# Optimization experiments

Measured on AMD Instinct MI355X. Metric: run time of the kernel, lower is better.

## Reference

```python
import jax, jax.numpy as jnp
import numpy as np

B, N, F = 4, 1024, 512        # batch, tokens, features
H, D = 8, 64                  # heads, attention_dim (= value dim here)
E = 16                        # edge feature dim
LN_EPS = 1e-5


def setup_inputs() -> dict:
    key = jax.random.key(0)
    ks = jax.random.split(key, 9)
    receiver_input = jax.random.normal(ks[0], (B, N, F), dtype=jnp.float32)
    edge_features = jax.random.normal(ks[1], (B, N, N, E), dtype=jnp.float32)
    mask = (jax.random.uniform(ks[2], (B, N, N)) > 0.5).astype(jnp.float32)
    s = 1.0 / np.sqrt(F)
    Wq = jax.random.normal(ks[3], (F, H * D), dtype=jnp.float32) * s
    Wk = jax.random.normal(ks[4], (F, H * D), dtype=jnp.float32) * s
    Wv = jax.random.normal(ks[5], (F, H * D), dtype=jnp.float32) * s
    We = jax.random.normal(ks[6], (E, H), dtype=jnp.float32) * (1.0 / np.sqrt(E))
    Wo = jax.random.normal(ks[7], (H * D, H * D), dtype=jnp.float32) * (1.0 / np.sqrt(H * D))
    ln_scale = jnp.ones((F,), dtype=jnp.float32)
    ln_offset = jnp.zeros((F,), dtype=jnp.float32)
    return {
        "receiver_input": receiver_input, "edge_features": edge_features,
        "mask": mask, "ln_scale": ln_scale, "ln_offset": ln_offset,
        "Wq": Wq, "Wk": Wk, "Wv": Wv, "We": We, "Wo": Wo,
    }


def _layer_norm(x, scale, offset):
    mu = jnp.mean(x, axis=-1, keepdims=True)
    var = jnp.var(x, axis=-1, keepdims=True)
    return (x - mu) * jax.lax.rsqrt(var + LN_EPS) * scale + offset


def reference(receiver_input, edge_features, mask, ln_scale, ln_offset, Wq, Wk, Wv, We, Wo):
    r = _layer_norm(receiver_input, ln_scale, ln_offset)   # sender = receiver (self-attn)
    q = (r @ Wq).reshape(B, N, H, D)
    k = (r @ Wk).reshape(B, N, H, D)
    v = (r @ Wv).reshape(B, N, H, D)
    # logits [b, i, j, h]; edge bias added BEFORE softmax (over senders j = axis -2)
    logits = jnp.einsum("bihf,bjhf->bijh", q, k) + edge_features @ We
    w = jax.nn.softmax(logits, axis=-2)
    w = w * mask[..., None]                                 # post-softmax mask multiply
    out = jnp.einsum("bijh,bjhv->bihv", w, v)
    out = out.reshape(B, N, H * D) * (1.0 / jnp.sqrt(jnp.float32(D)))
    out = out @ Wo
    out = out + receiver_input                              # residual (shapes match: F == H*D)
    return out
```

## Files before the change

### kernel.cpp

```cpp
#include <hip/hip_runtime.h>

#define BB 4
#define NN 1024
#define FF 512
#define HH 8
#define DD 64
#define EE 16

typedef unsigned short u16;
typedef __attribute__((ext_vector_type(8))) short     bf16x8;
typedef __attribute__((ext_vector_type(8))) unsigned short u16x8;
typedef __attribute__((ext_vector_type(4))) float     f32x4;

#define MFMA(a,b,c) __builtin_amdgcn_mfma_f32_16x16x32_bf16((a),(b),(c),0,0,0)

static __device__ __forceinline__ u16 f2bf(float f){
  unsigned u = __float_as_uint(f);
  unsigned r = (u + 0x7FFFu + ((u >> 16) & 1u)) >> 16;
  return (u16)r;
}
static __device__ __forceinline__ float bf2f(u16 h){
  return __uint_as_float(((unsigned)h) << 16);
}
static __device__ __forceinline__ void gld16(const void* g, void* l){
  __builtin_amdgcn_global_load_lds((const __attribute__((address_space(1))) unsigned int*)g,
                                   (__attribute__((address_space(3))) unsigned int*)l, 16, 0, 0);
}

__global__ __launch_bounds__(256) void k_wsplit(
    const float* __restrict__ Wq, const float* __restrict__ Wk,
    const float* __restrict__ Wv, const float* __restrict__ Wo,
    u16* __restrict__ WhT, u16* __restrict__ WlT, u16* __restrict__ WoT){
  __shared__ float tile[32][33];
  int bid = blockIdx.x, t = threadIdx.x;
  int isA = bid < 768;
  int tb  = isA ? bid : bid - 768;
  int nct = isA ? 48 : 16;
  int ct = tb % nct, ft = tb / nct;
  int c0 = ct * 32, f0 = ft * 32;
  #pragma unroll
  for (int r4 = 0; r4 < 4; r4++){
    int fl = (t >> 5) * 4 + r4, cl = t & 31;
    int f = f0 + fl, c = c0 + cl;
    float v;
    if (isA){
      const float* W = (c < 512) ? Wq : ((c < 1024) ? Wk : Wv);
      v = W[f * 512 + (c & 511)];
    } else {
      v = Wo[f * 512 + c];
    }
    tile[fl][cl] = v;
  }
  __syncthreads();
  #pragma unroll
  for (int r4 = 0; r4 < 4; r4++){
    int cl = (t >> 5) * 4 + r4, fl = t & 31;
    float v = tile[fl][cl];
    int c = c0 + cl, f = f0 + fl;
    if (isA){
      u16 hi = f2bf(v);
      WhT[c * 512 + f] = hi;
      WlT[c * 512 + f] = f2bf(v - bf2f(hi));
    } else {
      WoT[c * 512 + f] = f2bf(v);
    }
  }
}

__global__ __launch_bounds__(256) void k_ln(
    const float* __restrict__ x, const float* __restrict__ gamma,
    const float* __restrict__ beta, u16* __restrict__ rh, u16* __restrict__ rl){
  int row  = blockIdx.x * 4 + (threadIdx.x >> 6);
  int lane = threadIdx.x & 63;
  const float* px = x + (size_t)row * 512 + lane * 8;
  float4 a = *(const float4*)px;
  float4 b = *(const float4*)(px + 4);
  float v[8] = {a.x,a.y,a.z,a.w,b.x,b.y,b.z,b.w};
  float s = 0.f, q = 0.f;
  #pragma unroll
  for (int j = 0; j < 8; j++){ s += v[j]; q += v[j]*v[j]; }
  #pragma unroll
  for (int m = 1; m < 64; m <<= 1){ s += __shfl_xor(s, m, 64); q += __shfl_xor(q, m, 64); }
  float mean = s * (1.f/512.f);
  float var  = q * (1.f/512.f) - mean * mean;
  float rstd = rsqrtf(var + 1e-5f);
  float4 ga = *(const float4*)(gamma + lane*8);
  float4 gb = *(const float4*)(gamma + lane*8 + 4);
  float4 b0 = *(const float4*)(beta  + lane*8);
  float4 b1 = *(const float4*)(beta  + lane*8 + 4);
  float gs[8] = {ga.x,ga.y,ga.z,ga.w,gb.x,gb.y,gb.z,gb.w};
  float bs[8] = {b0.x,b0.y,b0.z,b0.w,b1.x,b1.y,b1.z,b1.w};
  u16x8 hv, lv;
  #pragma unroll
  for (int j = 0; j < 8; j++){
    float r = (v[j] - mean) * rstd * gs[j] + bs[j];
    u16 hi = f2bf(r);
    hv[j] = hi;
    lv[j] = f2bf(r - bf2f(hi));
  }
  *(u16x8*)(rh + (size_t)row * 512 + lane * 8) = hv;
  *(u16x8*)(rl + (size_t)row * 512 + lane * 8) = lv;
}

__global__ __launch_bounds__(256) void k_qkv(
    const u16* __restrict__ rh, const u16* __restrict__ rl,
    const u16* __restrict__ WhT, const u16* __restrict__ WlT,
    u16* __restrict__ qh, u16* __restrict__ ql,
    u16* __restrict__ kh, u16* __restrict__ kl, u16* __restrict__ vT){
  __shared__ u16 Ah[128*32], Al[128*32], Bh[128*32], Bl[128*32];
  int bid = blockIdx.x;
  int mt = bid & 31, nt = bid >> 5;
  int m0 = mt << 7,  n0 = nt << 7;
  int t = threadIdx.x, lane = t & 63, w = t >> 6;
  int wm = (w >> 1) << 6, wn = (w & 1) << 6;
  int fr = lane & 15, g = lane >> 4;
  f32x4 acc[4][4];
  #pragma unroll
  for (int i = 0; i < 4; i++)
    #pragma unroll
    for (int j = 0; j < 4; j++) acc[i][j] = (f32x4){0.f,0.f,0.f,0.f};

  for (int k0 = 0; k0 < 512; k0 += 32){
    #pragma unroll
    for (int q = 0; q < 2; q++){
      int c = ((q << 2) + w) * 64 + lane;
      int row = c >> 2, part = c & 3;
      int ldso = ((q << 2) + w) * 512;
      gld16(rh  + (size_t)(m0+row)*512 + k0 + part*8, &Ah[ldso]);
      gld16(rl  + (size_t)(m0+row)*512 + k0 + part*8, &Al[ldso]);
      gld16(WhT + (size_t)(n0+row)*512 + k0 + part*8, &Bh[ldso]);
      gld16(WlT + (size_t)(n0+row)*512 + k0 + part*8, &Bl[ldso]);
    }
    __syncthreads();
    bf16x8 a_h[4], a_l[4], b_h[4], b_l[4];
    #pragma unroll
    for (int mi = 0; mi < 4; mi++){
      int off = (wm + mi*16 + fr)*32 + g*8;
      a_h[mi] = *(const bf16x8*)&Ah[off];
      a_l[mi] = *(const bf16x8*)&Al[off];
    }
    #pragma unroll
    for (int ni = 0; ni < 4; ni++){
      int off = (wn + ni*16 + fr)*32 + g*8;
      b_h[ni] = *(const bf16x8*)&Bh[off];
      b_l[ni] = *(const bf16x8*)&Bl[off];
    }
    #pragma unroll
    for (int mi = 0; mi < 4; mi++)
      #pragma unroll
      for (int ni = 0; ni < 4; ni++){
        acc[mi][ni] = MFMA(a_h[mi], b_h[ni], acc[mi][ni]);
        acc[mi][ni] = MFMA(a_h[mi], b_l[ni], acc[mi][ni]);
        acc[mi][ni] = MFMA(a_l[mi], b_h[ni], acc[mi][ni]);
      }
    __syncthreads();
  }
  #pragma unroll
  for (int mi = 0; mi < 4; mi++)
    #pragma unroll
    for (int ni = 0; ni < 4; ni++)
      #pragma unroll
      for (int r = 0; r < 4; r++){
        int gm = m0 + wm + mi*16 + g*4 + r;
        int gc = n0 + wn + ni*16 + fr;
        float vv = acc[mi][ni][r];
        int b = gm >> 10, i = gm & 1023;
        int mat = gc >> 9, h = (gc >> 6) & 7, d = gc & 63;
        size_t idx = ((size_t)((b << 3) + h) * 1024 + i) * 64 + d;
        if (mat == 0){
          u16 hi = f2bf(vv); qh[idx] = hi; ql[idx] = f2bf(vv - bf2f(hi));
        } else if (mat == 1){
          u16 hi = f2bf(vv); kh[idx] = hi; kl[idx] = f2bf(vv - bf2f(hi));
        } else {
          vT[((size_t)((b << 3) + h) * 64 + d) * 1024 + i] = f2bf(vv);
        }
      }
}

__global__ __launch_bounds__(512) void k_attn(
    const float* __restrict__ edge, const float* __restrict__ mask,
    const float* __restrict__ We,
    const u16* __restrict__ qh, const u16* __restrict__ ql,
    const u16* __restrict__ kh, const u16* __restrict__ kl,
    const u16* __restrict__ vT, u16* __restrict__ AO){
  __shared__ float We_s[128];
  __shared__ float bias_s[8][16*33];
  __shared__ float mask_s[16*33];
  __shared__ u16   pm_s[8][16*40];

  int bid = blockIdx.x;
  int b = bid >> 6, i0 = (bid & 63) << 4;
  int t = threadIdx.x, lane = t & 63, w = t >> 6;
  int fr = lane & 15, g = lane >> 4;
  if (t < 128) We_s[t] = We[t];

  size_t qb = ((size_t)((b << 3) + w) * 1024 + i0 + fr) * 64 + g * 8;
  bf16x8 qfh0 = *(const bf16x8*)(qh + qb);
  bf16x8 qfh1 = *(const bf16x8*)(qh + qb + 32);
  bf16x8 qfl0 = *(const bf16x8*)(ql + qb);
  bf16x8 qfl1 = *(const bf16x8*)(ql + qb + 32);

  f32x4 oacc[4];
  #pragma unroll
  for (int vf = 0; vf < 4; vf++) oacc[vf] = (f32x4){0.f,0.f,0.f,0.f};
  float mrun[4], den[4];
  #pragma unroll
  for (int r = 0; r < 4; r++){ mrun[r] = -3e38f; den[r] = 0.f; }

  int pi = t >> 5, pj = t & 31;
  const float* ebase = edge + (size_t)(b*1024 + i0 + pi) * 16384 + (size_t)pj * 16;
  const float* mbase = mask + (size_t)(b*1024 + i0 + pi) * 1024 + pj;
  __syncthreads();

  float4 e0 = *(const float4*)(ebase);
  float4 e1 = *(const float4*)(ebase + 4);
  float4 e2 = *(const float4*)(ebase + 8);
  float4 e3 = *(const float4*)(ebase + 12);
  float  mval = *mbase;

  #pragma unroll 1
  for (int jt = 0; jt < 32; jt++){
    int j0 = jt << 5;
    float ef[16] = {e0.x,e0.y,e0.z,e0.w, e1.x,e1.y,e1.z,e1.w,
                    e2.x,e2.y,e2.z,e2.w, e3.x,e3.y,e3.z,e3.w};
    float bias[8] = {0.f,0.f,0.f,0.f,0.f,0.f,0.f,0.f};
    #pragma unroll
    for (int e = 0; e < 16; e++){
      float ev = ef[e];
      #pragma unroll
      for (int h = 0; h < 8; h++) bias[h] += ev * We_s[e*8 + h];
    }
    #pragma unroll
    for (int h = 0; h < 8; h++) bias_s[h][pi*33 + pj] = bias[h];
    mask_s[pi*33 + pj] = mval;
    __syncthreads();

    if (jt < 31){
      const float* ep = ebase + (size_t)(j0 + 32) * 16;
      e0 = *(const float4*)(ep);
      e1 = *(const float4*)(ep + 4);
      e2 = *(const float4*)(ep + 8);
      e3 = *(const float4*)(ep + 12);
      mval = mbase[j0 + 32];
    }

    size_t kb0 = ((size_t)((b << 3) + w) * 1024 + j0 + fr) * 64 + g * 8;
    size_t kb1 = kb0 + 16 * 64;
    bf16x8 kfh00 = *(const bf16x8*)(kh + kb0);
    bf16x8 kfh01 = *(const bf16x8*)(kh + kb0 + 32);
    bf16x8 kfh10 = *(const bf16x8*)(kh + kb1);
    bf16x8 kfh11 = *(const bf16x8*)(kh + kb1 + 32);
    bf16x8 kfl00 = *(const bf16x8*)(kl + kb0);
    bf16x8 kfl01 = *(const bf16x8*)(kl + kb0 + 32);
    bf16x8 kfl10 = *(const bf16x8*)(kl + kb1);
    bf16x8 kfl11 = *(const bf16x8*)(kl + kb1 + 32);

    f32x4 lg0 = (f32x4){0.f,0.f,0.f,0.f};
    f32x4 lg1 = (f32x4){0.f,0.f,0.f,0.f};
    lg0 = MFMA(qfh0, kfh00, lg0); lg0 = MFMA(qfh1, kfh01, lg0);
    lg0 = MFMA(qfh0, kfl00, lg0); lg0 = MFMA(qfh1, kfl01, lg0);
    lg0 = MFMA(qfl0, kfh00, lg0); lg0 = MFMA(qfl1, kfh01, lg0);
    lg1 = MFMA(qfh0, kfh10, lg1); lg1 = MFMA(qfh1, kfh11, lg1);
    lg1 = MFMA(qfh0, kfl10, lg1); lg1 = MFMA(qfh1, kfl11, lg1);
    lg1 = MFMA(qfl0, kfh10, lg1); lg1 = MFMA(qfl1, kfh11, lg1);

    float tm[4];
    #pragma unroll
    for (int r = 0; r < 4; r++){
      int row = g*4 + r;
      lg0[r] += bias_s[w][row*33 + fr];
      lg1[r] += bias_s[w][row*33 + 16 + fr];
      tm[r] = fmaxf(lg0[r], lg1[r]);
    }
    #pragma unroll
    for (int mk = 1; mk < 16; mk <<= 1){
      #pragma unroll
      for (int r = 0; r < 4; r++) tm[r] = fmaxf(tm[r], __shfl_xor(tm[r], mk, 16));
    }
    float p0[4], p1[4], scl[4], ps[4];
    #pragma unroll
    for (int r = 0; r < 4; r++){
      float nm = fmaxf(mrun[r], tm[r]);
      scl[r] = exp2f((mrun[r] - nm) * 1.44269504089f);
      mrun[r] = nm;
      p0[r] = exp2f((lg0[r] - nm) * 1.44269504089f);
      p1[r] = exp2f((lg1[r] - nm) * 1.44269504089f);
      ps[r] = p0[r] + p1[r];
    }
    #pragma unroll
    for (int mk = 1; mk < 16; mk <<= 1){
      #pragma unroll
      for (int r = 0; r < 4; r++) ps[r] += __shfl_xor(ps[r], mk, 16);
    }
    #pragma unroll
    for (int r = 0; r < 4; r++) den[r] = den[r] * scl[r] + ps[r];
    #pragma unroll
    for (int vf = 0; vf < 4; vf++)
      #pragma unroll
      for (int r = 0; r < 4; r++) oacc[vf][r] *= scl[r];

    #pragma unroll
    for (int r = 0; r < 4; r++){
      int row = g*4 + r;
      pm_s[w][row*40 + fr]      = f2bf(p0[r] * mask_s[row*33 + fr]);
      pm_s[w][row*40 + 16 + fr] = f2bf(p1[r] * mask_s[row*33 + 16 + fr]);
    }
    asm volatile("s_waitcnt lgkmcnt(0)" ::: "memory");
    bf16x8 pa = *(const bf16x8*)&pm_s[w][fr*40 + g*8];
    #pragma unroll
    for (int vf = 0; vf < 4; vf++){
      const u16* vp = vT + ((size_t)((b << 3) + w) * 64 + vf*16 + fr) * 1024 + j0 + g*8;
      bf16x8 vfr = *(const bf16x8*)vp;
      oacc[vf] = MFMA(pa, vfr, oacc[vf]);
    }
    __syncthreads();
  }

  float id[4];
  #pragma unroll
  for (int r = 0; r < 4; r++) id[r] = 0.125f / den[r];
  #pragma unroll
  for (int vf = 0; vf < 4; vf++)
    #pragma unroll
    for (int r = 0; r < 4; r++){
      int row = g*4 + r, v = vf*16 + fr;
      AO[((size_t)(b*1024 + i0 + row)) * 512 + w*64 + v] = f2bf(oacc[vf][r] * id[r]);
    }
}

__global__ __launch_bounds__(256) void k_out(
    const u16* __restrict__ AO, const u16* __restrict__ WoT,
    const float* __restrict__ x, float* __restrict__ out){
  __shared__ u16 As[64*32], Bs[128*32];
  int bid = blockIdx.x;
  int mt = bid & 63, nt = bid >> 6;
  int m0 = mt << 6, n0 = nt << 7;
  int t = threadIdx.x, lane = t & 63, w = t >> 6;
  int wm = (w >> 1) << 5, wn = (w & 1) << 6;
  int fr = lane & 15, g = lane >> 4;
  f32x4 acc[2][4];
  #pragma unroll
  for (int i = 0; i < 2; i++)
    #pragma unroll
    for (int j = 0; j < 4; j++) acc[i][j] = (f32x4){0.f,0.f,0.f,0.f};

  for (int k0 = 0; k0 < 512; k0 += 32){
    {
      int row = t >> 2, part = t & 3;
      gld16(AO + (size_t)(m0+row)*512 + k0 + part*8, &As[w*512]);
    }
    #pragma unroll
    for (int q = 0; q < 2; q++){
      int c = ((q << 2) + w) * 64 + lane;
      int row = c >> 2, part = c & 3;
      gld16(WoT + (size_t)(n0+row)*512 + k0 + part*8, &Bs[((q<<2)+w)*512]);
    }
    __syncthreads();
    bf16x8 af[2], bf_[4];
    #pragma unroll
    for (int mi = 0; mi < 2; mi++) af[mi]  = *(const bf16x8*)&As[(wm + mi*16 + fr)*32 + g*8];
    #pragma unroll
    for (int ni = 0; ni < 4; ni++) bf_[ni] = *(const bf16x8*)&Bs[(wn + ni*16 + fr)*32 + g*8];
    #pragma unroll
    for (int mi = 0; mi < 2; mi++)
      #pragma unroll
      for (int ni = 0; ni < 4; ni++)
        acc[mi][ni] = MFMA(af[mi], bf_[ni], acc[mi][ni]);
    __syncthreads();
  }
  #pragma unroll
  for (int mi = 0; mi < 2; mi++)
    #pragma unroll
    for (int ni = 0; ni < 4; ni++)
      #pragma unroll
      for (int r = 0; r < 4; r++){
        size_t gm = m0 + wm + mi*16 + g*4 + r;
        size_t gn = n0 + wn + ni*16 + fr;
        out[gm*512 + gn] = acc[mi][ni][r] + x[gm*512 + gn];
      }
}

extern "C" void kernel_launch(void* const* d_in, const int* in_sizes, int n_in,
                              void* d_out, int out_size, void* d_ws, size_t ws_size,
                              hipStream_t stream){
  const float* xin   = (const float*)d_in[0];
  const float* edge  = (const float*)d_in[1];
  const float* mask  = (const float*)d_in[2];
  const float* gamma = (const float*)d_in[3];
  const float* beta  = (const float*)d_in[4];
  const float* Wq    = (const float*)d_in[5];
  const float* Wk    = (const float*)d_in[6];
  const float* Wv    = (const float*)d_in[7];
  const float* We    = (const float*)d_in[8];
  const float* Wo    = (const float*)d_in[9];
  float* out = (float*)d_out;

  u16* p   = (u16*)d_ws;
  u16* WhT = p;                 p += 1536*512;
  u16* WlT = p;                 p += 1536*512;
  u16* WoT = p;                 p += 512*512;
  u16* rh  = p;                 p += 4096*512;
  u16* rl  = p;                 p += 4096*512;
  u16* qh  = p;                 p += 2097152;
  u16* ql  = p;                 p += 2097152;
  u16* kh  = p;                 p += 2097152;
  u16* kl  = p;                 p += 2097152;
  u16* vT  = p;                 p += 2097152;
  u16* AO  = p;                 p += 2097152;

  k_wsplit<<<1024, 256, 0, stream>>>(Wq, Wk, Wv, Wo, WhT, WlT, WoT);
  k_ln    <<<1024, 256, 0, stream>>>(xin, gamma, beta, rh, rl);
  k_qkv   <<<384,  256, 0, stream>>>(rh, rl, WhT, WlT, qh, ql, kh, kl, vT);
  k_attn  <<<256,  512, 0, stream>>>(edge, mask, We, qh, ql, kh, kl, vT, AO);
  k_out   <<<256,  256, 0, stream>>>(AO, WoT, xin, out);
}
```

Before: 215.1 us.

## Split attention over sender dimension with flash-decoding partials and combine kernel

The attention kernel now splits the 1024 senders into four chunks, launching four times as many blocks, and each writes a partial normalized output plus its running max and denominator. A new combine kernel merges the four partials with log-sum-exp weighting and writes the final attention output. It also adds an occupancy hint to launch bounds, interleaves the two independent MFMA chains, and reuses the workspace by aliasing the partials over the dead LN and weight buffers. The goal is better CU occupancy with 256 CUs, at the cost of an extra launch, extra partial traffic, and bf16 rounding of the partials.

```diff
diff --git a/kernel.cpp b/kernel.cpp
--- a/kernel.cpp
+++ b/kernel.cpp
@@ -177,19 +177,22 @@
       }
 }
 
-__global__ __launch_bounds__(512) void k_attn(
+__global__ __launch_bounds__(512, 6) void k_attn(
     const float* __restrict__ edge, const float* __restrict__ mask,
     const float* __restrict__ We,
     const u16* __restrict__ qh, const u16* __restrict__ ql,
     const u16* __restrict__ kh, const u16* __restrict__ kl,
-    const u16* __restrict__ vT, u16* __restrict__ AO){
+    const u16* __restrict__ vT, u16* __restrict__ part_o,
+    float2* __restrict__ part_md){
   __shared__ float We_s[128];
   __shared__ float bias_s[8][16*33];
   __shared__ float mask_s[16*33];
   __shared__ u16   pm_s[8][16*40];
 
   int bid = blockIdx.x;
-  int b = bid >> 6, i0 = (bid & 63) << 4;
+  int s  = bid & 3;
+  int i0 = ((bid >> 2) & 63) << 4;
+  int b  = bid >> 8;
   int t = threadIdx.x, lane = t & 63, w = t >> 6;
   int fr = lane & 15, g = lane >> 4;
   if (t < 128) We_s[t] = We[t];
@@ -208,8 +211,8 @@
   for (int r = 0; r < 4; r++){ mrun[r] = -3e38f; den[r] = 0.f; }
 
   int pi = t >> 5, pj = t & 31;
-  const float* ebase = edge + (size_t)(b*1024 + i0 + pi) * 16384 + (size_t)pj * 16;
-  const float* mbase = mask + (size_t)(b*1024 + i0 + pi) * 1024 + pj;
+  const float* ebase = edge + ((size_t)(b*1024 + i0 + pi) * 1024 + s*256 + pj) * 16;
+  const float* mbase = mask + (size_t)(b*1024 + i0 + pi) * 1024 + s*256 + pj;
   __syncthreads();
 
   float4 e0 = *(const float4*)(ebase);
@@ -219,8 +222,8 @@
   float  mval = *mbase;
 
   #pragma unroll 1
-  for (int jt = 0; jt < 32; jt++){
-    int j0 = jt << 5;
+  for (int jt = 0; jt < 8; jt++){
+    int j0 = s*256 + (jt << 5);
     float ef[16] = {e0.x,e0.y,e0.z,e0.w, e1.x,e1.y,e1.z,e1.w,
                     e2.x,e2.y,e2.z,e2.w, e3.x,e3.y,e3.z,e3.w};
     float bias[8] = {0.f,0.f,0.f,0.f,0.f,0.f,0.f,0.f};
@@ -235,13 +238,13 @@
     mask_s[pi*33 + pj] = mval;
     __syncthreads();
 
-    if (jt < 31){
-      const float* ep = ebase + (size_t)(j0 + 32) * 16;
+    if (jt < 7){
+      const float* ep = ebase + (size_t)((jt + 1) << 5) * 16;
       e0 = *(const float4*)(ep);
       e1 = *(const float4*)(ep + 4);
       e2 = *(const float4*)(ep + 8);
       e3 = *(const float4*)(ep + 12);
-      mval = mbase[j0 + 32];
+      mval = mbase[(jt + 1) << 5];
     }
 
     size_t kb0 = ((size_t)((b << 3) + w) * 1024 + j0 + fr) * 64 + g * 8;
@@ -257,12 +260,12 @@
 
     f32x4 lg0 = (f32x4){0.f,0.f,0.f,0.f};
     f32x4 lg1 = (f32x4){0.f,0.f,0.f,0.f};
-    lg0 = MFMA(qfh0, kfh00, lg0); lg0 = MFMA(qfh1, kfh01, lg0);
-    lg0 = MFMA(qfh0, kfl00, lg0); lg0 = MFMA(qfh1, kfl01, lg0);
-    lg0 = MFMA(qfl0, kfh00, lg0); lg0 = MFMA(qfl1, kfh01, lg0);
-    lg1 = MFMA(qfh0, kfh10, lg1); lg1 = MFMA(qfh1, kfh11, lg1);
-    lg1 = MFMA(qfh0, kfl10, lg1); lg1 = MFMA(qfh1, kfl11, lg1);
-    lg1 = MFMA(qfl0, kfh10, lg1); lg1 = MFMA(qfl1, kfh11, lg1);
+    lg0 = MFMA(qfh0, kfh00, lg0); lg1 = MFMA(qfh0, kfh10, lg1);
+    lg0 = MFMA(qfh1, kfh01, lg0); lg1 = MFMA(qfh1, kfh11, lg1);
+    lg0 = MFMA(qfh0, kfl00, lg0); lg1 = MFMA(qfh0, kfl10, lg1);
+    lg0 = MFMA(qfh1, kfl01, lg0); lg1 = MFMA(qfh1, kfl11, lg1);
+    lg0 = MFMA(qfl0, kfh00, lg0); lg1 = MFMA(qfl0, kfh10, lg1);
+    lg0 = MFMA(qfl1, kfh01, lg0); lg1 = MFMA(qfl1, kfh11, lg1);
 
     float tm[4];
     #pragma unroll
@@ -318,14 +321,47 @@
 
   float id[4];
   #pragma unroll
-  for (int r = 0; r < 4; r++) id[r] = 0.125f / den[r];
+  for (int r = 0; r < 4; r++) id[r] = 1.0f / den[r];
+  int bh = (b << 3) + w;
   #pragma unroll
   for (int vf = 0; vf < 4; vf++)
     #pragma unroll
     for (int r = 0; r < 4; r++){
-      int row = g*4 + r, v = vf*16 + fr;
-      AO[((size_t)(b*1024 + i0 + row)) * 512 + w*64 + v] = f2bf(oacc[vf][r] * id[r]);
-    }
+      int row = g*4 + r;
+      part_o[((size_t)((s*32 + bh) * 1024) + i0 + row) * 64 + vf*16 + fr] =
+          f2bf(oacc[vf][r] * id[r]);
+    }
+  if (fr == 0){
+    #pragma unroll
+    for (int r = 0; r < 4; r++){
+      int row = g*4 + r;
+      part_md[(size_t)(s*32 + bh) * 1024 + i0 + row] = make_float2(mrun[r], den[r]);
+    }
+  }
+}
+
+__global__ __launch_bounds__(256) void k_combine(
+    const u16* __restrict__ part_o, const float2* __restrict__ part_md,
+    u16* __restrict__ AO){
+  int wg   = blockIdx.x * 4 + (threadIdx.x >> 6);
+  int lane = threadIdx.x & 63;
+  int bh = wg >> 10, i = wg & 1023;
+  int b = bh >> 3, h = bh & 7;
+  float2 md[4];
+  float M = -3e38f;
+  #pragma unroll
+  for (int s = 0; s < 4; s++){
+    md[s] = part_md[(size_t)(s*32 + bh) * 1024 + i];
+    M = fmaxf(M, md[s].x);
+  }
+  float wsum = 0.f, o = 0.f;
+  #pragma unroll
+  for (int s = 0; s < 4; s++){
+    float wq = md[s].y * exp2f((md[s].x - M) * 1.44269504089f);
+    wsum += wq;
+    o += wq * bf2f(part_o[((size_t)((s*32 + bh) * 1024) + i) * 64 + lane]);
+  }
+  AO[((size_t)(b*1024 + i)) * 512 + h*64 + lane] = f2bf(o * 0.125f / wsum);
 }
 
 __global__ __launch_bounds__(256) void k_out(
@@ -396,21 +432,25 @@
   float* out = (float*)d_out;
 
   u16* p   = (u16*)d_ws;
-  u16* WhT = p;                 p += 1536*512;
-  u16* WlT = p;                 p += 1536*512;
   u16* WoT = p;                 p += 512*512;
-  u16* rh  = p;                 p += 4096*512;
-  u16* rl  = p;                 p += 4096*512;
   u16* qh  = p;                 p += 2097152;
   u16* ql  = p;                 p += 2097152;
   u16* kh  = p;                 p += 2097152;
   u16* kl  = p;                 p += 2097152;
   u16* vT  = p;                 p += 2097152;
   u16* AO  = p;                 p += 2097152;
-
-  k_wsplit<<<1024, 256, 0, stream>>>(Wq, Wk, Wv, Wo, WhT, WlT, WoT);
-  k_ln    <<<1024, 256, 0, stream>>>(xin, gamma, beta, rh, rl);
-  k_qkv   <<<384,  256, 0, stream>>>(rh, rl, WhT, WlT, qh, ql, kh, kl, vT);
-  k_attn  <<<256,  512, 0, stream>>>(edge, mask, We, qh, ql, kh, kl, vT, AO);
-  k_out   <<<256,  256, 0, stream>>>(AO, WoT, xin, out);
-}
+  u16* U   = p;
+  u16* rh  = U;
+  u16* rl  = U + 2097152;
+  u16* WhT = U + 4194304;
+  u16* WlT = U + 4194304 + 786432;
+  u16* part_o = U;
+  float2* part_md = (float2*)(U + 8388608);
+
+  k_wsplit <<<1024, 256, 0, stream>>>(Wq, Wk, Wv, Wo, WhT, WlT, WoT);
+  k_ln     <<<1024, 256, 0, stream>>>(xin, gamma, beta, rh, rl);
+  k_qkv    <<<384,  256, 0, stream>>>(rh, rl, WhT, WlT, qh, ql, kh, kl, vT);
+  k_attn   <<<1024, 512, 0, stream>>>(edge, mask, We, qh, ql, kh, kl, vT, part_o, part_md);
+  k_combine<<<8192, 256, 0, stream>>>(part_o, part_md, AO);
+  k_out    <<<256,  256, 0, stream>>>(AO, WoT, xin, out);
+}
```

Result: slower. 438.8 us (+104.0%).

## Double-buffer edge bias tiles and prefetch V fragments in attention loop

Applied to the files above, without the earlier changes.

The edge-bias and mask shared-memory tiles are double-buffered, so the bias for the next key tile is computed at the end of the current iteration. This removes one of the two block barriers per iteration. V fragments are now loaded at the start of each iteration alongside K, and sched_barriers pin the order in which the K/V and edge loads are issued. The hi/lo MFMA chains for the two logit tiles are interleaved to increase instruction-level parallelism. The cost is more shared memory and higher register pressure.

```diff
diff --git a/kernel.cpp b/kernel.cpp
--- a/kernel.cpp
+++ b/kernel.cpp
@@ -184,8 +184,8 @@
     const u16* __restrict__ kh, const u16* __restrict__ kl,
     const u16* __restrict__ vT, u16* __restrict__ AO){
   __shared__ float We_s[128];
-  __shared__ float bias_s[8][16*33];
-  __shared__ float mask_s[16*33];
+  __shared__ float bias_s[2][8][16*33];
+  __shared__ float mask_s[2][16*33];
   __shared__ u16   pm_s[8][16*40];
 
   int bid = blockIdx.x;
@@ -208,41 +208,35 @@
   for (int r = 0; r < 4; r++){ mrun[r] = -3e38f; den[r] = 0.f; }
 
   int pi = t >> 5, pj = t & 31;
-  const float* ebase = edge + (size_t)(b*1024 + i0 + pi) * 16384 + (size_t)pj * 16;
+  const float* ebase = edge + ((size_t)(b*1024 + i0 + pi) * 1024 + pj) * 16;
   const float* mbase = mask + (size_t)(b*1024 + i0 + pi) * 1024 + pj;
-  __syncthreads();
 
   float4 e0 = *(const float4*)(ebase);
   float4 e1 = *(const float4*)(ebase + 4);
   float4 e2 = *(const float4*)(ebase + 8);
   float4 e3 = *(const float4*)(ebase + 12);
   float  mval = *mbase;
+  __syncthreads();
+  {
+    float ef[16] = {e0.x,e0.y,e0.z,e0.w, e1.x,e1.y,e1.z,e1.w,
+                    e2.x,e2.y,e2.z,e2.w, e3.x,e3.y,e3.z,e3.w};
+    float bias[8] = {0.f,0.f,0.f,0.f,0.f,0.f,0.f,0.f};
+    #pragma unroll
+    for (int e = 0; e < 16; e++){
+      float ev = ef[e];
+      #pragma unroll
+      for (int h = 0; h < 8; h++) bias[h] += ev * We_s[e*8 + h];
+    }
+    #pragma unroll
+    for (int h = 0; h < 8; h++) bias_s[0][h][pi*33 + pj] = bias[h];
+    mask_s[0][pi*33 + pj] = mval;
+  }
+  __syncthreads();
+  int cur = 0;
 
   #pragma unroll 1
   for (int jt = 0; jt < 32; jt++){
     int j0 = jt << 5;
-    float ef[16] = {e0.x,e0.y,e0.z,e0.w, e1.x,e1.y,e1.z,e1.w,
-                    e2.x,e2.y,e2.z,e2.w, e3.x,e3.y,e3.z,e3.w};
-    float bias[8] = {0.f,0.f,0.f,0.f,0.f,0.f,0.f,0.f};
-    #pragma unroll
-    for (int e = 0; e < 16; e++){
-      float ev = ef[e];
-      #pragma unroll
-      for (int h = 0; h < 8; h++) bias[h] += ev * We_s[e*8 + h];
-    }
-    #pragma unroll
-    for (int h = 0; h < 8; h++) bias_s[h][pi*33 + pj] = bias[h];
-    mask_s[pi*33 + pj] = mval;
-    __syncthreads();
-
-    if (jt < 31){
-      const float* ep = ebase + (size_t)(j0 + 32) * 16;
-      e0 = *(const float4*)(ep);
-      e1 = *(const float4*)(ep + 4);
-      e2 = *(const float4*)(ep + 8);
-      e3 = *(const float4*)(ep + 12);
-      mval = mbase[j0 + 32];
-    }
 
     size_t kb0 = ((size_t)((b << 3) + w) * 1024 + j0 + fr) * 64 + g * 8;
     size_t kb1 = kb0 + 16 * 64;
@@ -254,22 +248,46 @@
     bf16x8 kfl01 = *(const bf16x8*)(kl + kb0 + 32);
     bf16x8 kfl10 = *(const bf16x8*)(kl + kb1);
     bf16x8 kfl11 = *(const bf16x8*)(kl + kb1 + 32);
+    bf16x8 vfr[4];
+    #pragma unroll
+    for (int vf = 0; vf < 4; vf++)
+      vfr[vf] = *(const bf16x8*)(vT + ((size_t)((b << 3) + w) * 64 + vf*16 + fr) * 1024 + j0 + g*8);
+    __builtin_amdgcn_sched_barrier(0);
+
+    if (jt < 31){
+      const float* ep = ebase + (size_t)(j0 + 32) * 16;
+      e0 = *(const float4*)(ep);
+      e1 = *(const float4*)(ep + 4);
+      e2 = *(const float4*)(ep + 8);
+      e3 = *(const float4*)(ep + 12);
+      mval = mbase[j0 + 32];
+    }
+    __builtin_amdgcn_sched_barrier(0);
+
+    float bs0[4], bs1[4], ms0[4], ms1[4];
+    #pragma unroll
+    for (int r = 0; r < 4; r++){
+      int row = g*4 + r;
+      bs0[r] = bias_s[cur][w][row*33 + fr];
+      bs1[r] = bias_s[cur][w][row*33 + 16 + fr];
+      ms0[r] = mask_s[cur][row*33 + fr];
+      ms1[r] = mask_s[cur][row*33 + 16 + fr];
+    }
 
     f32x4 lg0 = (f32x4){0.f,0.f,0.f,0.f};
     f32x4 lg1 = (f32x4){0.f,0.f,0.f,0.f};
-    lg0 = MFMA(qfh0, kfh00, lg0); lg0 = MFMA(qfh1, kfh01, lg0);
-    lg0 = MFMA(qfh0, kfl00, lg0); lg0 = MFMA(qfh1, kfl01, lg0);
-    lg0 = MFMA(qfl0, kfh00, lg0); lg0 = MFMA(qfl1, kfh01, lg0);
-    lg1 = MFMA(qfh0, kfh10, lg1); lg1 = MFMA(qfh1, kfh11, lg1);
-    lg1 = MFMA(qfh0, kfl10, lg1); lg1 = MFMA(qfh1, kfl11, lg1);
-    lg1 = MFMA(qfl0, kfh10, lg1); lg1 = MFMA(qfl1, kfh11, lg1);
+    lg0 = MFMA(qfh0, kfh00, lg0); lg1 = MFMA(qfh0, kfh10, lg1);
+    lg0 = MFMA(qfh1, kfh01, lg0); lg1 = MFMA(qfh1, kfh11, lg1);
+    lg0 = MFMA(qfh0, kfl00, lg0); lg1 = MFMA(qfh0, kfl10, lg1);
+    lg0 = MFMA(qfh1, kfl01, lg0); lg1 = MFMA(qfh1, kfl11, lg1);
+    lg0 = MFMA(qfl0, kfh00, lg0); lg1 = MFMA(qfl0, kfh10, lg1);
+    lg0 = MFMA(qfl1, kfh01, lg0); lg1 = MFMA(qfl1, kfh11, lg1);
 
     float tm[4];
     #pragma unroll
     for (int r = 0; r < 4; r++){
-      int row = g*4 + r;
-      lg0[r] += bias_s[w][row*33 + fr];
-      lg1[r] += bias_s[w][row*33 + 16 + fr];
+      lg0[r] += bs0[r];
+      lg1[r] += bs1[r];
       tm[r] = fmaxf(lg0[r], lg1[r]);
     }
     #pragma unroll
@@ -302,18 +320,32 @@
     #pragma unroll
     for (int r = 0; r < 4; r++){
       int row = g*4 + r;
-      pm_s[w][row*40 + fr]      = f2bf(p0[r] * mask_s[row*33 + fr]);
-      pm_s[w][row*40 + 16 + fr] = f2bf(p1[r] * mask_s[row*33 + 16 + fr]);
+      pm_s[w][row*40 + fr]      = f2bf(p0[r] * ms0[r]);
+      pm_s[w][row*40 + 16 + fr] = f2bf(p1[r] * ms1[r]);
     }
     asm volatile("s_waitcnt lgkmcnt(0)" ::: "memory");
     bf16x8 pa = *(const bf16x8*)&pm_s[w][fr*40 + g*8];
     #pragma unroll
-    for (int vf = 0; vf < 4; vf++){
-      const u16* vp = vT + ((size_t)((b << 3) + w) * 64 + vf*16 + fr) * 1024 + j0 + g*8;
-      bf16x8 vfr = *(const bf16x8*)vp;
-      oacc[vf] = MFMA(pa, vfr, oacc[vf]);
+    for (int vf = 0; vf < 4; vf++)
+      oacc[vf] = MFMA(pa, vfr[vf], oacc[vf]);
+
+    if (jt < 31){
+      float ef[16] = {e0.x,e0.y,e0.z,e0.w, e1.x,e1.y,e1.z,e1.w,
+                      e2.x,e2.y,e2.z,e2.w, e3.x,e3.y,e3.z,e3.w};
+      float bias[8] = {0.f,0.f,0.f,0.f,0.f,0.f,0.f,0.f};
+      #pragma unroll
+      for (int e = 0; e < 16; e++){
+        float ev = ef[e];
+        #pragma unroll
+        for (int h = 0; h < 8; h++) bias[h] += ev * We_s[e*8 + h];
+      }
+      int nxt = cur ^ 1;
+      #pragma unroll
+      for (int h = 0; h < 8; h++) bias_s[nxt][h][pi*33 + pj] = bias[h];
+      mask_s[nxt][pi*33 + pj] = mval;
     }
     __syncthreads();
+    cur ^= 1;
   }
 
   float id[4];
```

Result: slower. 220.0 us (+2.3%).
